# Optimization experiments

Measured on AMD Instinct MI355X. Metric: run time of the kernel, lower is better.

## Reference

```python
import jax, jax.numpy as jnp
import numpy as np

D_MODEL = 1024
N_HEAD = 16
D_HEAD = D_MODEL // N_HEAD
N_EXPERTS = 8
TOP_K = 2
D_FF = 4096
EPS = 1e-6


def setup_inputs() -> dict:
    key = jax.random.key(0)
    ks = jax.random.split(key, 16)
    s = 0.02  # init scale
    d, dff, E = D_MODEL, D_FF, N_EXPERTS
    return {
        "dec": jax.random.normal(ks[0], (4, 1024, d), jnp.float32),
        "text_encoder": jax.random.normal(ks[1], (4, 512, d), jnp.float32),
        # self-attention projections
        "Wq1": jax.random.normal(ks[2], (d, d), jnp.float32) * s,
        "Wk1": jax.random.normal(ks[3], (d, d), jnp.float32) * s,
        "Wv1": jax.random.normal(ks[4], (d, d), jnp.float32) * s,
        "Wo1": jax.random.normal(ks[5], (d, d), jnp.float32) * s,
        # cross-attention projections
        "Wq2": jax.random.normal(ks[6], (d, d), jnp.float32) * s,
        "Wk2": jax.random.normal(ks[7], (d, d), jnp.float32) * s,
        "Wv2": jax.random.normal(ks[8], (d, d), jnp.float32) * s,
        "Wo2": jax.random.normal(ks[9], (d, d), jnp.float32) * s,
        # shared RMSNorm gain (module uses one norm instance three times)
        "g": jnp.ones((d,), jnp.float32),
        # MoE router + per-expert FFN weights
        "Wg": jax.random.normal(ks[10], (d, E), jnp.float32) * s,
        "W1": jax.random.normal(ks[11], (E, d, dff), jnp.float32) * s,
        "W2": jax.random.normal(ks[12], (E, dff, d), jnp.float32) * s,
    }


def rmsnorm(x, g):
    return x * jax.lax.rsqrt(jnp.mean(x * x, axis=-1, keepdims=True) + EPS) * g


def mha(q_in, k_in, v_in, Wq, Wk, Wv, Wo):
    B, Sq, _ = q_in.shape
    Sk = k_in.shape[1]
    q = (q_in @ Wq).reshape(B, Sq, N_HEAD, D_HEAD)
    k = (k_in @ Wk).reshape(B, Sk, N_HEAD, D_HEAD)
    v = (v_in @ Wv).reshape(B, Sk, N_HEAD, D_HEAD)
    scores = jnp.einsum("bqhd,bkhd->bhqk", q, k) / jnp.sqrt(jnp.asarray(D_HEAD, q.dtype))
    attn = jax.nn.softmax(scores, axis=-1)
    out = jnp.einsum("bhqk,bkhd->bqhd", attn, v).reshape(B, Sq, D_MODEL)
    return out @ Wo


def moe(x, Wg, W1, W2):
    # top-k softmax router, renormalized weights; dense per-expert FFN with combine
    probs = jax.nn.softmax(x @ Wg, axis=-1)              # [B,S,E]
    weights, indices = jax.lax.top_k(probs, TOP_K)        # [B,S,k]
    weights = weights / jnp.sum(weights, axis=-1, keepdims=True)
    # combine[t,e] = sum_k weights[t,k] * (indices[t,k]==e)
    combine = jnp.sum(
        jax.nn.one_hot(indices, N_EXPERTS, dtype=x.dtype) * weights[..., None], axis=-2
    )  # [B,S,E]
    out = jnp.zeros_like(x)
    for e in range(N_EXPERTS):  # fixed small expert loop
        h = jax.nn.relu(x @ W1[e]) @ W2[e]
        out = out + combine[..., e:e + 1] * h
    return weights, indices, out


def reference(dec, text_encoder, Wq1, Wk1, Wv1, Wo1, Wq2, Wk2, Wv2, Wo2, g, Wg, W1, W2):
    # self-attention + residual + RMSNorm (dropout p=0 -> identity)
    x = rmsnorm(mha(dec, dec, dec, Wq1, Wk1, Wv1, Wo1) + dec, g)
    # cross-attention + residual + RMSNorm
    x = rmsnorm(mha(x, text_encoder, text_encoder, Wq2, Wk2, Wv2, Wo2) + x, g)
    # MoE FFN + residual + RMSNorm
    weights, indices, y = moe(x, Wg, W1, W2)
    x = rmsnorm(y + x, g)
    return weights, indices, x
```

## Files before the change

### kernel.cpp

```cpp
#include <hip/hip_runtime.h>
#include <stdint.h>

#define D_    1024
#define BB    4
#define SDEC  1024
#define STXT  512
#define TDEC  4096
#define TTXT  2048
#define NH    16
#define DHD   64
#define NE    8
#define DFF   4096
#define NSLOT 8192
#define ND1   8192
#define ND2   4096
#define MOEGRID 512

using u16 = unsigned short;
typedef __attribute__((ext_vector_type(8))) short bf16x8;
typedef __attribute__((ext_vector_type(4))) float f32x4;

__device__ __forceinline__ float bf2f(u16 h) {
    union { unsigned int u; float f; } x; x.u = ((unsigned int)h) << 16; return x.f;
}
__device__ __forceinline__ u16 f2bf(float f) {
    union { float f; unsigned int u; } x; x.f = f;
    unsigned int lsb = (x.u >> 16) & 1u;
    return (u16)((x.u + 0x7fffu + lsb) >> 16);
}

__device__ __forceinline__ void gld16(const u16* g, u16* l) {
    __builtin_amdgcn_global_load_lds((const __attribute__((address_space(1))) void*)g,
                                     (__attribute__((address_space(3))) void*)l,
                                     16, 0, 0);
}

template<int EPI>
__global__ __launch_bounds__(256) void proj_k64(
    const u16* __restrict__ AH, const u16* __restrict__ AL,
    const u16* __restrict__ BH, const u16* __restrict__ BL,
    float* __restrict__ Cf, u16* __restrict__ CH, u16* __restrict__ CL,
    int M, int N, int ldc)
{
    __shared__ u16 smem[24576];
    u16* sAH = smem;
    u16* sAL = smem + 8192;
    u16* sBH = smem + 16384;
    u16* sBL = smem + 20480;

    const int tileM = blockIdx.y * 128, tileN = blockIdx.x * 64;
    const int t = threadIdx.x;
    const int srow = t >> 3;
    const int scol = ((t & 7) ^ (srow & 7)) << 3;
    const u16* pA  = AH + (long)(tileM + srow) * 1024 + scol;
    const u16* pAl = AL + (long)(tileM + srow) * 1024 + scol;
    const u16* pB  = BH + (long)(tileN + srow) * 1024 + scol;
    const u16* pBl = BL + (long)(tileN + srow) * 1024 + scol;

    const int lane = t & 63, wv = t >> 6;
    const int wr = wv << 5;
    const int fr = lane & 15, kg = lane >> 4;

    f32x4 acc[2][4];
    const f32x4 vzero = {0.f, 0.f, 0.f, 0.f};
#pragma unroll
    for (int m = 0; m < 2; ++m)
#pragma unroll
        for (int n = 0; n < 4; ++n) acc[m][n] = vzero;

    for (int rr = 0; rr < 16; ++rr) {
        const long k0 = (long)rr << 6;
#pragma unroll
        for (int c = 0; c < 4; ++c) {
            const long ro = 32L * c * 1024;
            gld16(pA  + k0 + ro, sAH + c * 2048 + t * 8);
            gld16(pAl + k0 + ro, sAL + c * 2048 + t * 8);
        }
#pragma unroll
        for (int c = 0; c < 2; ++c) {
            const long ro = 32L * c * 1024;
            gld16(pB  + k0 + ro, sBH + c * 2048 + t * 8);
            gld16(pBl + k0 + ro, sBL + c * 2048 + t * 8);
        }
        __syncthreads();

#pragma unroll
        for (int ks = 0; ks < 2; ++ks) {
            bf16x8 fa[2], fb[4], fal[2], fbl[4];
#pragma unroll
            for (int m = 0; m < 2; ++m) {
                const int r = wr + m * 16 + fr;
                const int o = r * 64 + (((kg | (ks << 2)) ^ (r & 7)) << 3);
                fa[m]  = *(const bf16x8*)&sAH[o];
                fal[m] = *(const bf16x8*)&sAL[o];
            }
#pragma unroll
            for (int n = 0; n < 4; ++n) {
                const int r = n * 16 + fr;
                const int o = r * 64 + (((kg | (ks << 2)) ^ (r & 7)) << 3);
                fb[n]  = *(const bf16x8*)&sBH[o];
                fbl[n] = *(const bf16x8*)&sBL[o];
            }
#pragma unroll
            for (int m = 0; m < 2; ++m)
#pragma unroll
                for (int n = 0; n < 4; ++n) {
                    acc[m][n] = __builtin_amdgcn_mfma_f32_16x16x32_bf16(fa[m],  fb[n],  acc[m][n], 0, 0, 0);
                    acc[m][n] = __builtin_amdgcn_mfma_f32_16x16x32_bf16(fa[m],  fbl[n], acc[m][n], 0, 0, 0);
                    acc[m][n] = __builtin_amdgcn_mfma_f32_16x16x32_bf16(fal[m], fb[n],  acc[m][n], 0, 0, 0);
                }
        }
        __syncthreads();
    }

#pragma unroll
    for (int m = 0; m < 2; ++m) {
        const int r0 = tileM + wr + m * 16 + (kg << 2);
#pragma unroll
        for (int n = 0; n < 4; ++n) {
            const int col = tileN + n * 16 + fr;
#pragma unroll
            for (int i = 0; i < 4; ++i) {
                const float v = acc[m][n][i];
                const long off = (long)(r0 + i) * ldc + col;
                if constexpr (EPI == 0) {
                    Cf[off] = v;
                } else {
                    const u16 h = f2bf(v);
                    CH[off] = h;
                    CL[off] = f2bf(v - bf2f(h));
                }
            }
        }
    }
}

__global__ __launch_bounds__(256) void scores_k64(
    const u16* __restrict__ AH, const u16* __restrict__ AL,
    const u16* __restrict__ BH, const u16* __restrict__ BL,
    u16* __restrict__ CH, u16* __restrict__ CL,
    int lda, int ldb, int ldc, int nb2,
    long strA1, long strA2, long strB1, long strB2, long strC1, long strC2)
{
    __shared__ u16 smem[4 * 8192];
    u16* sAH = smem;
    u16* sAL = smem + 8192;
    u16* sBH = smem + 16384;
    u16* sBL = smem + 24576;

    const int z = blockIdx.z;
    const int z1 = z / nb2, z2 = z % nb2;
    const long zA = (long)z1 * strA1 + (long)z2 * strA2;
    const long zB = (long)z1 * strB1 + (long)z2 * strB2;
    const long zC = (long)z1 * strC1 + (long)z2 * strC2;

    const int tileM = blockIdx.y * 128, tileN = blockIdx.x * 128;
    const int t = threadIdx.x;
    const int srow = t >> 3;
    const int scol = ((t & 7) ^ (srow & 7)) << 3;
    const u16* pA  = AH + zA + (long)(tileM + srow) * lda + scol;
    const u16* pAl = AL + zA + (long)(tileM + srow) * lda + scol;
    const u16* pB  = BH + zB + (long)(tileN + srow) * ldb + scol;
    const u16* pBl = BL + zB + (long)(tileN + srow) * ldb + scol;

#pragma unroll
    for (int c = 0; c < 4; ++c) {
        const long ro = 32L * c * lda;
        const long rb = 32L * c * ldb;
        gld16(pA  + ro, sAH + c * 2048 + t * 8);
        gld16(pAl + ro, sAL + c * 2048 + t * 8);
        gld16(pB  + rb, sBH + c * 2048 + t * 8);
        gld16(pBl + rb, sBL + c * 2048 + t * 8);
    }
    __syncthreads();

    const int lane = t & 63;
    const int wv = t >> 6;
    const int wr = (wv >> 1) << 6, wc = (wv & 1) << 6;
    const int fr = lane & 15, kg = lane >> 4;

    f32x4 acc[4][4];
    const f32x4 vzero = {0.f, 0.f, 0.f, 0.f};
#pragma unroll
    for (int m = 0; m < 4; ++m)
#pragma unroll
        for (int n = 0; n < 4; ++n) acc[m][n] = vzero;

#pragma unroll
    for (int ks = 0; ks < 2; ++ks) {
        bf16x8 fa[4], fb[4], fal[4], fbl[4];
#pragma unroll
        for (int m = 0; m < 4; ++m) {
            const int r = wr + m * 16 + fr;
            const int o = r * 64 + (((kg | (ks << 2)) ^ (r & 7)) << 3);
            fa[m]  = *(const bf16x8*)&sAH[o];
            fal[m] = *(const bf16x8*)&sAL[o];
        }
#pragma unroll
        for (int n = 0; n < 4; ++n) {
            const int r = wc + n * 16 + fr;
            const int o = r * 64 + (((kg | (ks << 2)) ^ (r & 7)) << 3);
            fb[n]  = *(const bf16x8*)&sBH[o];
            fbl[n] = *(const bf16x8*)&sBL[o];
        }
#pragma unroll
        for (int m = 0; m < 4; ++m)
#pragma unroll
            for (int n = 0; n < 4; ++n) {
                acc[m][n] = __builtin_amdgcn_mfma_f32_16x16x32_bf16(fa[m],  fb[n],  acc[m][n], 0, 0, 0);
                acc[m][n] = __builtin_amdgcn_mfma_f32_16x16x32_bf16(fa[m],  fbl[n], acc[m][n], 0, 0, 0);
                acc[m][n] = __builtin_amdgcn_mfma_f32_16x16x32_bf16(fal[m], fb[n],  acc[m][n], 0, 0, 0);
            }
    }

#pragma unroll
    for (int m = 0; m < 4; ++m) {
        const int r0 = tileM + wr + m * 16 + (kg << 2);
#pragma unroll
        for (int n = 0; n < 4; ++n) {
            const int col = tileN + wc + n * 16 + fr;
#pragma unroll
            for (int i = 0; i < 4; ++i) {
                const float v = acc[m][n][i];
                const long off = zC + (long)(r0 + i) * ldc + col;
                const u16 h = f2bf(v);
                CH[off] = h;
                CL[off] = f2bf(v - bf2f(h));
            }
        }
    }
}

__global__ __launch_bounds__(256) void pv_k64(
    const u16* __restrict__ PHp, const u16* __restrict__ PLp,
    const u16* __restrict__ VTH, const u16* __restrict__ VTL,
    float* __restrict__ Op, int Skv, int NZ)
{
    __shared__ u16 smem[24576];
    u16* sAH = smem;
    u16* sAL = smem + 8192;
    u16* sBH = smem + 16384;
    u16* sBL = smem + 20480;

    const int kq = blockIdx.x;
    const int tileM = blockIdx.y * 128;
    const int z = blockIdx.z;
    const int kbase = kq * (Skv >> 2);
    const int nrounds = Skv >> 8;

    const int t = threadIdx.x;
    const int srow = t >> 3;
    const int scol = ((t & 7) ^ (srow & 7)) << 3;
    const u16* pA  = PHp + (long)z * 1024 * Skv + (long)(tileM + srow) * Skv + kbase + scol;
    const u16* pAl = PLp + (long)z * 1024 * Skv + (long)(tileM + srow) * Skv + kbase + scol;
    const u16* pB  = VTH + (long)z * 64 * Skv + (long)srow * Skv + kbase + scol;
    const u16* pBl = VTL + (long)z * 64 * Skv + (long)srow * Skv + kbase + scol;

    const int lane = t & 63, wv = t >> 6;
    const int wr = wv << 5;
    const int fr = lane & 15, kg = lane >> 4;

    f32x4 acc[2][4];
    const f32x4 vzero = {0.f, 0.f, 0.f, 0.f};
#pragma unroll
    for (int m = 0; m < 2; ++m)
#pragma unroll
        for (int n = 0; n < 4; ++n) acc[m][n] = vzero;

    for (int rr = 0; rr < nrounds; ++rr) {
        const long k0 = (long)rr << 6;
#pragma unroll
        for (int c = 0; c < 4; ++c) {
            const long ro = 32L * c * Skv;
            gld16(pA  + k0 + ro, sAH + c * 2048 + t * 8);
            gld16(pAl + k0 + ro, sAL + c * 2048 + t * 8);
        }
#pragma unroll
        for (int c = 0; c < 2; ++c) {
            const long ro = 32L * c * Skv;
            gld16(pB  + k0 + ro, sBH + c * 2048 + t * 8);
            gld16(pBl + k0 + ro, sBL + c * 2048 + t * 8);
        }
        __syncthreads();

#pragma unroll
        for (int ks = 0; ks < 2; ++ks) {
            bf16x8 fa[2], fb[4], fal[2], fbl[4];
#pragma unroll
            for (int m = 0; m < 2; ++m) {
                const int r = wr + m * 16 + fr;
                const int o = r * 64 + (((kg | (ks << 2)) ^ (r & 7)) << 3);
                fa[m]  = *(const bf16x8*)&sAH[o];
                fal[m] = *(const bf16x8*)&sAL[o];
            }
#pragma unroll
            for (int n = 0; n < 4; ++n) {
                const int r = n * 16 + fr;
                const int o = r * 64 + (((kg | (ks << 2)) ^ (r & 7)) << 3);
                fb[n]  = *(const bf16x8*)&sBH[o];
                fbl[n] = *(const bf16x8*)&sBL[o];
            }
#pragma unroll
            for (int m = 0; m < 2; ++m)
#pragma unroll
                for (int n = 0; n < 4; ++n) {
                    acc[m][n] = __builtin_amdgcn_mfma_f32_16x16x32_bf16(fa[m],  fb[n],  acc[m][n], 0, 0, 0);
                    acc[m][n] = __builtin_amdgcn_mfma_f32_16x16x32_bf16(fa[m],  fbl[n], acc[m][n], 0, 0, 0);
                    acc[m][n] = __builtin_amdgcn_mfma_f32_16x16x32_bf16(fal[m], fb[n],  acc[m][n], 0, 0, 0);
                }
        }
        __syncthreads();
    }

    const long base = ((long)kq * NZ + z) * 65536;
#pragma unroll
    for (int m = 0; m < 2; ++m) {
        const int r0 = tileM + wr + m * 16 + (kg << 2);
#pragma unroll
        for (int n = 0; n < 4; ++n) {
            const int col = n * 16 + fr;
#pragma unroll
            for (int i = 0; i < 4; ++i)
                Op[base + (long)(r0 + i) * 64 + col] = acc[m][n][i];
        }
    }
}

__global__ __launch_bounds__(256) void pv_combine(
    const float* __restrict__ Op, u16* __restrict__ aoH, u16* __restrict__ aoL,
    int nz, int nh)
{
    const long i = ((long)blockIdx.x * 256 + threadIdx.x) * 4;
    const int zz = (int)(i >> 16);
    const int rem = (int)(i & 65535);
    const int r = rem >> 6, c = rem & 63;
    const int b = zz / nh, h = zz % nh;
    const long kqS = (long)nz * 65536;
    float4 v = *(const float4*)(Op + i);
    const float4 v1 = *(const float4*)(Op + kqS + i);
    const float4 v2 = *(const float4*)(Op + 2 * kqS + i);
    const float4 v3 = *(const float4*)(Op + 3 * kqS + i);
    v.x += v1.x + v2.x + v3.x;
    v.y += v1.y + v2.y + v3.y;
    v.z += v1.z + v2.z + v3.z;
    v.w += v1.w + v2.w + v3.w;
    const long dst = (long)b * SDEC * D_ + (long)r * D_ + h * 64 + c;
    u16 h0 = f2bf(v.x), h1 = f2bf(v.y), h2 = f2bf(v.z), h3 = f2bf(v.w);
    uint2 hh;
    hh.x = (unsigned)h0 | ((unsigned)h1 << 16);
    hh.y = (unsigned)h2 | ((unsigned)h3 << 16);
    *(uint2*)(aoH + dst) = hh;
    u16 l0 = f2bf(v.x - bf2f(h0)), l1 = f2bf(v.y - bf2f(h1));
    u16 l2 = f2bf(v.z - bf2f(h2)), l3 = f2bf(v.w - bf2f(h3));
    uint2 ll;
    ll.x = (unsigned)l0 | ((unsigned)l1 << 16);
    ll.y = (unsigned)l2 | ((unsigned)l3 << 16);
    *(uint2*)(aoL + dst) = ll;
}

template<int EPI>
__global__ __launch_bounds__(256, 2) void moe_gemm2(
    const u16* __restrict__ Ag, int lda,
    const u16* __restrict__ BTbase, int ldb, long btStride,
    float* __restrict__ Cf0, float* __restrict__ Cf1, u16* __restrict__ CH, int ldc,
    const int4* __restrict__ desc, int ndesc, int Kiter)
{
    __shared__ u16 smem[32768];
    const int t = threadIdx.x;
    const int lane = t & 63, wv = t >> 6;
    const int wr = (wv >> 1) << 6, wc = (wv & 1) << 6;
    const int fr = lane & 15, kg = lane >> 4;
    const int nks = Kiter >> 5;

    const int rS = t >> 2;
    const int cS = ((t & 3) ^ ((t >> 3) & 3)) << 3;

    int ldsA[4], ldsB[4];
#pragma unroll
    for (int m = 0; m < 4; ++m) {
        const int ra = wr + m * 16 + fr;
        ldsA[m] = ra * 32 + ((kg ^ ((ra >> 1) & 3)) << 3);
        const int rb = wc + m * 16 + fr;
        ldsB[m] = rb * 32 + ((kg ^ ((rb >> 1) & 3)) << 3);
    }

    for (int p = blockIdx.x; p < ndesc; p += MOEGRID) {
        const int4 d = desc[p];
        if (d.x < 0) continue;
        const int rowbase = d.x, colbase = d.y & 0xFFFF, e = d.y >> 16;
        const int kbase = d.z, s1 = d.w;
        const u16* paS = Ag + (long)(rowbase + rS) * lda + kbase + cS;
        const u16* pbS = BTbase + (long)e * btStride + (long)(colbase + rS) * ldb + kbase + cS;
        const long hA = 64L * lda, hB = 64L * ldb;

        f32x4 acc[4][4];
        const f32x4 vzero = {0.f, 0.f, 0.f, 0.f};
#pragma unroll
        for (int m = 0; m < 4; ++m)
#pragma unroll
            for (int n = 0; n < 4; ++n) acc[m][n] = vzero;

#define STG(ks) { const int s_ = (ks) & 3; const long k0_ = (long)(ks) << 5; \
        u16* b_ = smem + s_ * 8192; \
        gld16(paS + k0_,      b_ + t * 8); \
        gld16(paS + k0_ + hA, b_ + 2048 + t * 8); \
        gld16(pbS + k0_,      b_ + 4096 + t * 8); \
        gld16(pbS + k0_ + hB, b_ + 6144 + t * 8); }

        STG(0); STG(1); STG(2);
        asm volatile("s_waitcnt vmcnt(8)" ::: "memory");
        __builtin_amdgcn_s_barrier();
        __builtin_amdgcn_sched_barrier(0);

        for (int ks = 0; ks < nks; ++ks) {
            if (ks + 3 < nks) STG(ks + 3);
            const u16* sA = smem + (ks & 3) * 8192;
            const u16* sB = sA + 4096;
            bf16x8 fa[4], fb[4];
#pragma unroll
            for (int m = 0; m < 4; ++m) fa[m] = *(const bf16x8*)&sA[ldsA[m]];
#pragma unroll
            for (int n = 0; n < 4; ++n) fb[n] = *(const bf16x8*)&sB[ldsB[n]];
            __builtin_amdgcn_s_setprio(1);
#pragma unroll
            for (int m = 0; m < 4; ++m)
#pragma unroll
                for (int n = 0; n < 4; ++n)
                    acc[m][n] = __builtin_amdgcn_mfma_f32_16x16x32_bf16(fa[m], fb[n], acc[m][n], 0, 0, 0);
            __builtin_amdgcn_s_setprio(0);
            if (ks + 3 < nks)      { asm volatile("s_waitcnt vmcnt(8)" ::: "memory"); }
            else if (ks + 2 < nks) { asm volatile("s_waitcnt vmcnt(4)" ::: "memory"); }
            else                   { asm volatile("s_waitcnt vmcnt(0)" ::: "memory"); }
            __builtin_amdgcn_s_barrier();
            __builtin_amdgcn_sched_barrier(0);
        }
#undef STG

        float* __restrict__ C = (EPI == 0) ? ((kbase == 0) ? Cf0 : Cf1) : nullptr;
#pragma unroll
        for (int m = 0; m < 4; ++m) {
            const int r0 = rowbase + wr + m * 16 + (kg << 2);
#pragma unroll
            for (int n = 0; n < 4; ++n) {
                const int col = colbase + wc + n * 16 + fr;
#pragma unroll
                for (int i = 0; i < 4; ++i) {
                    const int r = r0 + i;
                    if (r >= s1) continue;
                    const float v = acc[m][n][i];
                    const long off = (long)r * ldc + col;
                    if constexpr (EPI == 0) C[off] = v;
                    else                    CH[off] = f2bf(fmaxf(v, 0.f));
                }
            }
        }
    }
}

__global__ __launch_bounds__(256) void split2k(const float* __restrict__ in,
                                               u16* __restrict__ oh, u16* __restrict__ ol, long n)
{
    long i = ((long)blockIdx.x * 256 + threadIdx.x) * 4;
    if (i >= n) return;
    float4 v = *(const float4*)(in + i);
    u16 h0 = f2bf(v.x), h1 = f2bf(v.y), h2 = f2bf(v.z), h3 = f2bf(v.w);
    uint2 oo;
    oo.x = (unsigned)h0 | ((unsigned)h1 << 16);
    oo.y = (unsigned)h2 | ((unsigned)h3 << 16);
    *(uint2*)(oh + i) = oo;
    if (ol) {
        u16 l0 = f2bf(v.x - bf2f(h0)), l1 = f2bf(v.y - bf2f(h1));
        u16 l2 = f2bf(v.z - bf2f(h2)), l3 = f2bf(v.w - bf2f(h3));
        uint2 ll;
        ll.x = (unsigned)l0 | ((unsigned)l1 << 16);
        ll.y = (unsigned)l2 | ((unsigned)l3 << 16);
        *(uint2*)(ol + i) = ll;
    }
}

struct Ptr8 { const float* p[8]; };
__global__ __launch_bounds__(256) void transpose_split_w(
    Ptr8 in, u16* __restrict__ oh, u16* __restrict__ ol)
{
    __shared__ float tile[32][33];
    const int z = blockIdx.z;
    const float* ip = in.p[z];
    u16* ohp = oh + (long)z * D_ * D_;
    u16* olp = ol + (long)z * D_ * D_;
    const int c0 = blockIdx.x * 32, r0 = blockIdx.y * 32;
    const int tx = threadIdx.x & 31, ty = threadIdx.x >> 5;
    for (int i = ty; i < 32; i += 8)
        tile[i][tx] = ip[(long)(r0 + i) * D_ + c0 + tx];
    __syncthreads();
    for (int i = ty; i < 32; i += 8) {
        int oc = c0 + i, orr = r0 + tx;
        float v = tile[tx][i];
        u16 h = f2bf(v);
        ohp[(long)oc * D_ + orr] = h;
        olp[(long)oc * D_ + orr] = f2bf(v - bf2f(h));
    }
}

__global__ __launch_bounds__(256) void transpose_split(
    const float* __restrict__ in, u16* __restrict__ oh, u16* __restrict__ ol,
    int R, int C, int ild, long ibs1, long ibs2, int nb2, int old_, long obs)
{
    __shared__ float tile[32][33];
    const int z = blockIdx.z;
    const float* ip = in + (long)(z / nb2) * ibs1 + (long)(z % nb2) * ibs2;
    u16* ohp = oh + (long)z * obs;
    u16* olp = ol ? ol + (long)z * obs : nullptr;
    const int c0 = blockIdx.x * 32, r0 = blockIdx.y * 32;
    const int tx = threadIdx.x & 31, ty = threadIdx.x >> 5;
    for (int i = ty; i < 32; i += 8) {
        int r = r0 + i, c = c0 + tx;
        tile[i][tx] = (r < R && c < C) ? ip[(long)r * ild + c] : 0.f;
    }
    __syncthreads();
    for (int i = ty; i < 32; i += 8) {
        int oc = c0 + i, orr = r0 + tx;
        if (oc < C && orr < R) {
            float v = tile[tx][i];
            u16 h = f2bf(v);
            ohp[(long)oc * old_ + orr] = h;
            if (olp) olp[(long)oc * old_ + orr] = f2bf(v - bf2f(h));
        }
    }
}

__global__ __launch_bounds__(256) void transpose_split_hl(
    const u16* __restrict__ inH, const u16* __restrict__ inL,
    u16* __restrict__ oh, u16* __restrict__ ol,
    int R, int C, int ild, long ibs1, long ibs2, int nb2, int old_, long obs)
{
    __shared__ float tile[32][33];
    const int z = blockIdx.z;
    const long base = (long)(z / nb2) * ibs1 + (long)(z % nb2) * ibs2;
    u16* ohp = oh + (long)z * obs;
    u16* olp = ol + (long)z * obs;
    const int c0 = blockIdx.x * 32, r0 = blockIdx.y * 32;
    const int tx = threadIdx.x & 31, ty = threadIdx.x >> 5;
    for (int i = ty; i < 32; i += 8) {
        int r = r0 + i, c = c0 + tx;
        float v = 0.f;
        if (r < R && c < C) {
            const long o = base + (long)r * ild + c;
            v = bf2f(inH[o]) + bf2f(inL[o]);
        }
        tile[i][tx] = v;
    }
    __syncthreads();
    for (int i = ty; i < 32; i += 8) {
        int oc = c0 + i, orr = r0 + tx;
        if (oc < C && orr < R) {
            float v = tile[tx][i];
            u16 h = f2bf(v);
            ohp[(long)oc * old_ + orr] = h;
            olp[(long)oc * old_ + orr] = f2bf(v - bf2f(h));
        }
    }
}

__global__ __launch_bounds__(256) void softmax_hl(
    u16* __restrict__ ph, u16* __restrict__ pl, int cols, float scale)
{
    u16* php = ph + (long)blockIdx.x * cols;
    u16* plp = pl + (long)blockIdx.x * cols;
    const int t = threadIdx.x;
    float v[4];
    int vpt;
    if (cols == 1024) {
        vpt = 4;
        uint2 hh = ((const uint2*)php)[t];
        uint2 ll = ((const uint2*)plp)[t];
        v[0] = (bf2f((u16)(hh.x & 0xffff)) + bf2f((u16)(ll.x & 0xffff))) * scale;
        v[1] = (bf2f((u16)(hh.x >> 16))    + bf2f((u16)(ll.x >> 16)))    * scale;
        v[2] = (bf2f((u16)(hh.y & 0xffff)) + bf2f((u16)(ll.y & 0xffff))) * scale;
        v[3] = (bf2f((u16)(hh.y >> 16))    + bf2f((u16)(ll.y >> 16)))    * scale;
    } else {
        vpt = 2;
        unsigned hh = ((const unsigned*)php)[t];
        unsigned ll = ((const unsigned*)plp)[t];
        v[0] = (bf2f((u16)(hh & 0xffff)) + bf2f((u16)(ll & 0xffff))) * scale;
        v[1] = (bf2f((u16)(hh >> 16))    + bf2f((u16)(ll >> 16)))    * scale;
        v[2] = -3.4e38f; v[3] = -3.4e38f;
    }
    float mx = fmaxf(fmaxf(v[0], v[1]), fmaxf(v[2], v[3]));
#pragma unroll
    for (int o = 32; o; o >>= 1) mx = fmaxf(mx, __shfl_xor(mx, o));
    __shared__ float sm[4];
    const int wv = t >> 6, ln = t & 63;
    if (ln == 0) sm[wv] = mx;
    __syncthreads();
    mx = fmaxf(fmaxf(sm[0], sm[1]), fmaxf(sm[2], sm[3]));
    float sum = 0.f;
    for (int i = 0; i < vpt; ++i) { v[i] = expf(v[i] - mx); sum += v[i]; }
#pragma unroll
    for (int o = 32; o; o >>= 1) sum += __shfl_xor(sum, o);
    __shared__ float ss[4];
    if (ln == 0) ss[wv] = sum;
    __syncthreads();
    sum = ss[0] + ss[1] + ss[2] + ss[3];
    const float inv = 1.f / sum;
    if (cols == 1024) {
        float q0 = v[0] * inv, q1 = v[1] * inv, q2 = v[2] * inv, q3 = v[3] * inv;
        u16 h0 = f2bf(q0), h1 = f2bf(q1), h2 = f2bf(q2), h3 = f2bf(q3);
        uint2 hh; hh.x = (unsigned)h0 | ((unsigned)h1 << 16); hh.y = (unsigned)h2 | ((unsigned)h3 << 16);
        ((uint2*)php)[t] = hh;
        u16 l0 = f2bf(q0 - bf2f(h0)), l1 = f2bf(q1 - bf2f(h1));
        u16 l2 = f2bf(q2 - bf2f(h2)), l3 = f2bf(q3 - bf2f(h3));
        uint2 llo; llo.x = (unsigned)l0 | ((unsigned)l1 << 16); llo.y = (unsigned)l2 | ((unsigned)l3 << 16);
        ((uint2*)plp)[t] = llo;
    } else {
        float q0 = v[0] * inv, q1 = v[1] * inv;
        u16 h0 = f2bf(q0), h1 = f2bf(q1);
        ((unsigned*)php)[t] = (unsigned)h0 | ((unsigned)h1 << 16);
        u16 l0 = f2bf(q0 - bf2f(h0)), l1 = f2bf(q1 - bf2f(h1));
        ((unsigned*)plp)[t] = (unsigned)l0 | ((unsigned)l1 << 16);
    }
}

__global__ __launch_bounds__(256) void add_rmsnorm(
    const float* __restrict__ a, const float* __restrict__ b, const float* __restrict__ g,
    float* __restrict__ xo, u16* __restrict__ xh, u16* __restrict__ xl)
{
    const long row = blockIdx.x;
    const int t = threadIdx.x;
    const float* pa = a + row * D_;
    const float* pb = b + row * D_;
    float v[4]; double ssq = 0.0;
#pragma unroll
    for (int i = 0; i < 4; ++i) {
        int c = t + (i << 8);
        v[i] = pa[c] + pb[c];
        ssq += (double)v[i] * v[i];
    }
#pragma unroll
    for (int o = 32; o; o >>= 1) ssq += __shfl_xor(ssq, o);
    __shared__ double sd[4];
    if ((t & 63) == 0) sd[t >> 6] = ssq;
    __syncthreads();
    ssq = sd[0] + sd[1] + sd[2] + sd[3];
    const float rs = (float)(1.0 / sqrt(ssq * (1.0 / 1024.0) + 1e-6));
#pragma unroll
    for (int i = 0; i < 4; ++i) {
        int c = t + (i << 8);
        float o = v[i] * rs * g[c];
        xo[row * D_ + c] = o;
        if (xh) {
            u16 h = f2bf(o);
            xh[row * D_ + c] = h;
            if (xl) xl[row * D_ + c] = f2bf(o - bf2f(h));
        }
    }
}

__global__ __launch_bounds__(256) void router_topk(
    const float* __restrict__ x2, const float* __restrict__ Wg,
    float* __restrict__ outw, float* __restrict__ outi,
    int* __restrict__ idx, float* __restrict__ tokw, int* __restrict__ counts, int T)
{
    const int wid = (int)((blockIdx.x * 256 + threadIdx.x) >> 6);
    const int lane = threadIdx.x & 63;
    if (wid >= T) return;
    float acc[NE];
#pragma unroll
    for (int e = 0; e < NE; ++e) acc[e] = 0.f;
    const float* xr = x2 + (long)wid * D_;
    for (int i = 0; i < 16; ++i) {
        float xv = xr[i * 64 + lane];
        const float* wr = Wg + (long)(i * 64 + lane) * NE;
#pragma unroll
        for (int e = 0; e < NE; ++e) acc[e] += xv * wr[e];
    }
#pragma unroll
    for (int e = 0; e < NE; ++e)
#pragma unroll
        for (int o = 32; o; o >>= 1) acc[e] += __shfl_xor(acc[e], o);
    if (lane == 0) {
        float m = acc[0];
#pragma unroll
        for (int e = 1; e < NE; ++e) m = fmaxf(m, acc[e]);
        float p[NE], s = 0.f;
#pragma unroll
        for (int e = 0; e < NE; ++e) { p[e] = expf(acc[e] - m); s += p[e]; }
        const float invs = 1.f / s;
#pragma unroll
        for (int e = 0; e < NE; ++e) p[e] *= invs;
        int e0 = 0;
#pragma unroll
        for (int e = 1; e < NE; ++e) if (p[e] > p[e0]) e0 = e;
        int e1 = (e0 == 0) ? 1 : 0;
#pragma unroll
        for (int e = 0; e < NE; ++e) if (e != e0 && e != e1 && p[e] > p[e1]) e1 = e;
        float w0 = p[e0], w1 = p[e1];
        const float sw = 1.f / (w0 + w1);
        w0 *= sw; w1 *= sw;
        outw[2 * wid] = w0;      outw[2 * wid + 1] = w1;
        outi[2 * wid] = (float)e0; outi[2 * wid + 1] = (float)e1;
        idx[2 * wid] = e0;       idx[2 * wid + 1] = e1;
        tokw[2 * wid] = w0;      tokw[2 * wid + 1] = w1;
        atomicAdd(&counts[e0], 1);
        atomicAdd(&counts[e1], 1);
    }
}

__global__ void scan_desc(const int* __restrict__ counts, int* __restrict__ cursor,
                          int4* __restrict__ d1, int4* __restrict__ d2)
{
    __shared__ int sseg[NE + 1];
    if (threadIdx.x == 0) {
        int a = 0;
        for (int e = 0; e < NE; ++e) { sseg[e] = a; cursor[e] = a; a += counts[e]; }
        sseg[NE] = a;
    }
    __syncthreads();
    const int e = threadIdx.x;
    if (e < NE) {
        const int s0 = sseg[e], s1 = sseg[e + 1];
        const int nyt = (s1 - s0 + 127) >> 7;
        for (int xt = 0; xt < 32; ++xt)
            for (int yt = 0; yt < nyt; ++yt)
                d1[e + 8 * (xt * nyt + yt)] =
                    make_int4(s0 + yt * 128, (xt * 128) | (e << 16), 0, s1);
        for (int kh = 0; kh < 2; ++kh)
            for (int xt = 0; xt < 8; ++xt)
                for (int yt = 0; yt < nyt; ++yt)
                    d2[e + 8 * ((kh * 8 + xt) * nyt + yt)] =
                        make_int4(s0 + yt * 128, (xt * 128) | (e << 16), kh * 2048, s1);
    }
}

__global__ __launch_bounds__(256) void scatter_slots(
    const int* __restrict__ idx, int* __restrict__ cursor,
    int* __restrict__ row_token, int* __restrict__ slot_of, int T)
{
    const int t = blockIdx.x * 256 + threadIdx.x;
    if (t >= T) return;
#pragma unroll
    for (int k = 0; k < 2; ++k) {
        const int e = idx[2 * t + k];
        const int pos = atomicAdd(&cursor[e], 1);
        row_token[pos] = t;
        slot_of[2 * t + k] = pos;
    }
}

__global__ __launch_bounds__(256) void gather_bf16(
    const float* __restrict__ x2, const int* __restrict__ row_token, u16* __restrict__ Xg)
{
    const int r = blockIdx.x;
    const int t = threadIdx.x;
    const float* src = x2 + (long)row_token[r] * D_ + t * 4;
    float4 v = *(const float4*)src;
    uint2 oo;
    oo.x = (unsigned)f2bf(v.x) | ((unsigned)f2bf(v.y) << 16);
    oo.y = (unsigned)f2bf(v.z) | ((unsigned)f2bf(v.w) << 16);
    *(uint2*)(Xg + (long)r * D_ + t * 4) = oo;
}

__global__ __launch_bounds__(256) void combine_rmsnorm(
    const float* __restrict__ Y0, const float* __restrict__ Y1,
    const int* __restrict__ slot_of, const float* __restrict__ tokw,
    const float* __restrict__ x2, const float* __restrict__ g, float* __restrict__ out)
{
    const long tr = blockIdx.x;
    const int t = threadIdx.x;
    const int s0 = slot_of[2 * tr], s1 = slot_of[2 * tr + 1];
    const float w0 = tokw[2 * tr], w1 = tokw[2 * tr + 1];
    const float* ya0 = Y0 + (long)s0 * D_;
    const float* yb0 = Y1 + (long)s0 * D_;
    const float* ya1 = Y0 + (long)s1 * D_;
    const float* yb1 = Y1 + (long)s1 * D_;
    const float* xr = x2 + tr * D_;
    float v[4]; double ssq = 0.0;
#pragma unroll
    for (int i = 0; i < 4; ++i) {
        int c = t + (i << 8);
        v[i] = w0 * (ya0[c] + yb0[c]) + w1 * (ya1[c] + yb1[c]) + xr[c];
        ssq += (double)v[i] * v[i];
    }
#pragma unroll
    for (int o = 32; o; o >>= 1) ssq += __shfl_xor(ssq, o);
    __shared__ double sd[4];
    if ((t & 63) == 0) sd[t >> 6] = ssq;
    __syncthreads();
    ssq = sd[0] + sd[1] + sd[2] + sd[3];
    const float rs = (float)(1.0 / sqrt(ssq * (1.0 / 1024.0) + 1e-6));
#pragma unroll
    for (int i = 0; i < 4; ++i) {
        int c = t + (i << 8);
        out[tr * D_ + c] = v[i] * rs * g[c];
    }
}

__global__ void sentinel(float* o) { o[0] = 12345.0f; }

extern "C" void kernel_launch(void* const* d_in, const int* in_sizes, int n_in,
                              void* d_out, int out_size, void* d_ws, size_t ws_size,
                              hipStream_t stream)
{
    const float* dec = (const float*)d_in[0];
    const float* te  = (const float*)d_in[1];
    const float* g  = (const float*)d_in[10];
    const float* Wg = (const float*)d_in[11];
    const float* W1 = (const float*)d_in[12];
    const float* W2 = (const float*)d_in[13];
    float* outw = (float*)d_out;
    float* outi = outw + 2 * TDEC;
    float* outx = outw + 4 * TDEC;

    char* ws = (char*)d_ws;
    size_t off = 0;
    auto A = [&](size_t bytes) -> char* {
        char* p = ws + off;
        off += (bytes + 255) & ~(size_t)255;
        return p;
    };

    u16* decH = (u16*)A((size_t)TDEC * D_ * 2);
    u16* decL = (u16*)A((size_t)TDEC * D_ * 2);
    u16* teH  = (u16*)A((size_t)TTXT * D_ * 2);
    u16* teL  = (u16*)A((size_t)TTXT * D_ * 2);
    u16* wtHall = (u16*)A((size_t)8 * D_ * D_ * 2);
    u16* wtLall = (u16*)A((size_t)8 * D_ * D_ * 2);
    float* x1f = (float*)A((size_t)TDEC * D_ * 4);
    float* x2f = (float*)A((size_t)TDEC * D_ * 4);
    float* tokw = (float*)A(NSLOT * 4);
    int* idx    = (int*)A(NSLOT * 4);
    int* counts = (int*)A(256);
    int* cursor = (int*)A(256);
    int* row_token = (int*)A(NSLOT * 4);
    int* slot_of   = (int*)A(NSLOT * 4);
    int4* desc1 = (int4*)A((size_t)ND1 * 16);
    int4* desc2 = (int4*)A((size_t)ND2 * 16);
    const size_t Rbase = off;

    u16* W1T  = (u16*)A((size_t)NE * DFF * D_ * 2);
    u16* W2T  = (u16*)A((size_t)NE * D_ * DFF * 2);
    u16* Xg   = (u16*)A((size_t)(NSLOT + 256) * D_ * 2);
    u16* Hb   = (u16*)A((size_t)(NSLOT + 256) * DFF * 2);
    float* Yseg = (float*)A((size_t)NSLOT * D_ * 4);
    float* Ypart1 = (float*)W1T;
    const size_t moeEnd = off;

    auto allocAttn = [&](bool batched, u16*& PH, u16*& PL, u16*& qkvH, u16*& qkvL,
                         u16*& q2H, u16*& q2L, u16*& kv2H, u16*& kv2L,
                         u16*& vTH, u16*& vTL, u16*& aoH, u16*& aoL,
                         u16*& x1H, u16*& x1L, float*& of, float*& Opart) {
        off = Rbase;
        const size_t pcell = batched ? (size_t)BB * NH * SDEC * SDEC * 2
                                     : (size_t)NH * SDEC * SDEC * 2;
        PH = (u16*)A(pcell);
        PL = (u16*)A(pcell);
        qkvH = (u16*)A((size_t)TDEC * 3 * D_ * 2);
        qkvL = (u16*)A((size_t)TDEC * 3 * D_ * 2);
        q2H  = (u16*)A((size_t)TDEC * D_ * 2);
        q2L  = (u16*)A((size_t)TDEC * D_ * 2);
        kv2H = (u16*)A((size_t)TTXT * 2 * D_ * 2);
        kv2L = (u16*)A((size_t)TTXT * 2 * D_ * 2);
        vTH = (u16*)A((size_t)TDEC * D_ * 2);
        vTL = (u16*)A((size_t)TDEC * D_ * 2);
        aoH = (u16*)A((size_t)TDEC * D_ * 2);
        aoL = (u16*)A((size_t)TDEC * D_ * 2);
        x1H = (u16*)A((size_t)TDEC * D_ * 2);
        x1L = (u16*)A((size_t)TDEC * D_ * 2);
        of  = (float*)A((size_t)TDEC * D_ * 4);
        Opart = (float*)A((size_t)4 * (batched ? BB * NH : NH) * SDEC * DHD * 4);
        return off;
    };

    u16 *PH, *PL, *qkvH, *qkvL, *q2H, *q2L, *kv2H, *kv2L, *vTH, *vTL, *aoH, *aoL, *x1H, *x1L;
    float *of, *Opart;
    size_t attnEnd = allocAttn(true, PH, PL, qkvH, qkvL, q2H, q2L, kv2H, kv2L,
                               vTH, vTL, aoH, aoL, x1H, x1L, of, Opart);
    bool batched = ws_size >= (attnEnd > moeEnd ? attnEnd : moeEnd);
    if (!batched) {
        attnEnd = allocAttn(false, PH, PL, qkvH, qkvL, q2H, q2L, kv2H, kv2L,
                            vTH, vTL, aoH, aoL, x1H, x1L, of, Opart);
        if (ws_size < (attnEnd > moeEnd ? attnEnd : moeEnd)) {
            sentinel<<<1, 1, 0, stream>>>(outw);
            return;
        }
    }

    const dim3 blk(256);

    split2k<<<dim3((TDEC * D_) / 1024), blk, 0, stream>>>(dec, decH, decL, (long)TDEC * D_);
    split2k<<<dim3((TTXT * D_) / 1024), blk, 0, stream>>>(te, teH, teL, (long)TTXT * D_);
    Ptr8 wp;
    for (int i = 0; i < 8; ++i) wp.p[i] = (const float*)d_in[2 + i];
    transpose_split_w<<<dim3(32, 32, 8), blk, 0, stream>>>(wp, wtHall, wtLall);

    proj_k64<1><<<dim3(48, 32), blk, 0, stream>>>(decH, decL, wtHall, wtLall,
        nullptr, qkvH, qkvL, TDEC, 3 * D_, 3 * D_);
    transpose_split_hl<<<dim3(2, 32, BB * NH), blk, 0, stream>>>(qkvH + 2 * D_, qkvL + 2 * D_,
        vTH, vTL, SDEC, DHD, 3 * D_, (long)SDEC * 3 * D_, DHD, NH, SDEC, (long)DHD * SDEC);

    if (batched) {
        scores_k64<<<dim3(8, 8, BB * NH), blk, 0, stream>>>(
            qkvH, qkvL, qkvH + D_, qkvL + D_, PH, PL,
            3 * D_, 3 * D_, SDEC, NH,
            (long)SDEC * 3 * D_, DHD, (long)SDEC * 3 * D_, DHD,
            (long)NH * SDEC * SDEC, (long)SDEC * SDEC);
        softmax_hl<<<dim3(BB * NH * SDEC), blk, 0, stream>>>(PH, PL, SDEC, 0.125f);
        pv_k64<<<dim3(4, 8, BB * NH), blk, 0, stream>>>(PH, PL, vTH, vTL, Opart, SDEC, BB * NH);
        pv_combine<<<dim3(BB * NH * 64), blk, 0, stream>>>(Opart, aoH, aoL, BB * NH, NH);
    } else {
        for (int b = 0; b < BB; ++b) {
            const long qo3 = (long)b * SDEC * 3 * D_;
            const long qo  = (long)b * SDEC * D_;
            scores_k64<<<dim3(8, 8, NH), blk, 0, stream>>>(
                qkvH + qo3, qkvL + qo3, qkvH + qo3 + D_, qkvL + qo3 + D_,
                PH, PL, 3 * D_, 3 * D_, SDEC, NH,
                0, DHD, 0, DHD, 0, (long)SDEC * SDEC);
            softmax_hl<<<dim3(NH * SDEC), blk, 0, stream>>>(PH, PL, SDEC, 0.125f);
            pv_k64<<<dim3(4, 8, NH), blk, 0, stream>>>(PH, PL,
                vTH + (long)b * NH * DHD * SDEC, vTL + (long)b * NH * DHD * SDEC,
                Opart, SDEC, NH);
            pv_combine<<<dim3(NH * 64), blk, 0, stream>>>(Opart, aoH + qo, aoL + qo, NH, NH);
        }
    }
    proj_k64<0><<<dim3(16, 32), blk, 0, stream>>>(aoH, aoL,
        wtHall + (size_t)3 * D_ * D_, wtLall + (size_t)3 * D_ * D_,
        of, nullptr, nullptr, TDEC, D_, D_);
    add_rmsnorm<<<dim3(TDEC), blk, 0, stream>>>(of, dec, g, x1f, x1H, x1L);

    proj_k64<1><<<dim3(16, 32), blk, 0, stream>>>(x1H, x1L,
        wtHall + (size_t)4 * D_ * D_, wtLall + (size_t)4 * D_ * D_,
        nullptr, q2H, q2L, TDEC, D_, D_);
    proj_k64<1><<<dim3(32, 16), blk, 0, stream>>>(teH, teL,
        wtHall + (size_t)5 * D_ * D_, wtLall + (size_t)5 * D_ * D_,
        nullptr, kv2H, kv2L, TTXT, 2 * D_, 2 * D_);
    transpose_split_hl<<<dim3(2, 16, BB * NH), blk, 0, stream>>>(kv2H + D_, kv2L + D_,
        vTH, vTL, STXT, DHD, 2 * D_, (long)STXT * 2 * D_, DHD, NH, STXT, (long)DHD * STXT);

    if (batched) {
        scores_k64<<<dim3(4, 8, BB * NH), blk, 0, stream>>>(
            q2H, q2L, kv2H, kv2L, PH, PL,
            D_, 2 * D_, STXT, NH,
            (long)SDEC * D_, DHD, (long)STXT * 2 * D_, DHD,
            (long)NH * SDEC * STXT, (long)SDEC * STXT);
        softmax_hl<<<dim3(BB * NH * SDEC), blk, 0, stream>>>(PH, PL, STXT, 0.125f);
        pv_k64<<<dim3(4, 8, BB * NH), blk, 0, stream>>>(PH, PL, vTH, vTL, Opart, STXT, BB * NH);
        pv_combine<<<dim3(BB * NH * 64), blk, 0, stream>>>(Opart, aoH, aoL, BB * NH, NH);
    } else {
        for (int b = 0; b < BB; ++b) {
            const long qo  = (long)b * SDEC * D_;
            const long ko2 = (long)b * STXT * 2 * D_;
            scores_k64<<<dim3(4, 8, NH), blk, 0, stream>>>(
                q2H + qo, q2L + qo, kv2H + ko2, kv2L + ko2,
                PH, PL, D_, 2 * D_, STXT, NH,
                0, DHD, 0, DHD, 0, (long)SDEC * STXT);
            softmax_hl<<<dim3(NH * SDEC), blk, 0, stream>>>(PH, PL, STXT, 0.125f);
            pv_k64<<<dim3(4, 8, NH), blk, 0, stream>>>(PH, PL,
                vTH + (long)b * NH * DHD * STXT, vTL + (long)b * NH * DHD * STXT,
                Opart, STXT, NH);
            pv_combine<<<dim3(NH * 64), blk, 0, stream>>>(Opart, aoH + qo, aoL + qo, NH, NH);
        }
    }
    proj_k64<0><<<dim3(16, 32), blk, 0, stream>>>(aoH, aoL,
        wtHall + (size_t)7 * D_ * D_, wtLall + (size_t)7 * D_ * D_,
        of, nullptr, nullptr, TDEC, D_, D_);
    add_rmsnorm<<<dim3(TDEC), blk, 0, stream>>>(of, x1f, g, x2f, nullptr, nullptr);

    hipMemsetAsync(counts, 0, 32, stream);
    hipMemsetAsync(desc1, 0xFF, (size_t)ND1 * 16, stream);
    hipMemsetAsync(desc2, 0xFF, (size_t)ND2 * 16, stream);
    router_topk<<<dim3(TDEC / 4), blk, 0, stream>>>(x2f, Wg, outw, outi, idx, tokw, counts, TDEC);
    scan_desc<<<1, 64, 0, stream>>>(counts, cursor, desc1, desc2);
    scatter_slots<<<dim3(TDEC / 256), blk, 0, stream>>>(idx, cursor, row_token, slot_of, TDEC);
    gather_bf16<<<dim3(NSLOT), blk, 0, stream>>>(x2f, row_token, Xg);

    transpose_split<<<dim3(DFF / 32, D_ / 32, NE), blk, 0, stream>>>(W1, W1T, nullptr,
        D_, DFF, DFF, (long)D_ * DFF, 0, 1, D_, (long)DFF * D_);
    transpose_split<<<dim3(D_ / 32, DFF / 32, NE), blk, 0, stream>>>(W2, W2T, nullptr,
        DFF, D_, D_, (long)D_ * DFF, 0, 1, DFF, (long)D_ * DFF);
    moe_gemm2<2><<<dim3(MOEGRID), blk, 0, stream>>>(Xg, D_, W1T, D_, (long)DFF * D_,
        nullptr, nullptr, Hb, DFF, desc1, ND1, 1024);
    moe_gemm2<0><<<dim3(MOEGRID), blk, 0, stream>>>(Hb, DFF, W2T, DFF, (long)D_ * DFF,
        Yseg, Ypart1, nullptr, D_, desc2, ND2, 2048);
    combine_rmsnorm<<<dim3(TDEC), blk, 0, stream>>>(Yseg, Ypart1, slot_of, tokw, x2f, g, outx);

    (void)in_sizes; (void)n_in; (void)out_size;
}
```

Before: 1.245 ms.

## Replace 4-stage LDS pipeline in MoE GEMM with single-buffer 64-wide K rounds

```diff
diff --git a/kernel.cpp b/kernel.cpp
--- a/kernel.cpp
+++ b/kernel.cpp
@@ -14,7 +14,7 @@
 #define NSLOT 8192
 #define ND1   8192
 #define ND2   4096
-#define MOEGRID 512
+#define MOEGRID 1280
 
 using u16 = unsigned short;
 typedef __attribute__((ext_vector_type(8))) short bf16x8;
@@ -359,39 +359,32 @@
 }
 
 template<int EPI>
-__global__ __launch_bounds__(256, 2) void moe_gemm2(
+__global__ __launch_bounds__(256) void moe_gemm2(
     const u16* __restrict__ Ag, int lda,
     const u16* __restrict__ BTbase, int ldb, long btStride,
     float* __restrict__ Cf0, float* __restrict__ Cf1, u16* __restrict__ CH, int ldc,
     const int4* __restrict__ desc, int ndesc, int Kiter)
 {
-    __shared__ u16 smem[32768];
+    __shared__ u16 smem[16384];
+    u16* sA = smem;
+    u16* sB = smem + 8192;
+
     const int t = threadIdx.x;
     const int lane = t & 63, wv = t >> 6;
     const int wr = (wv >> 1) << 6, wc = (wv & 1) << 6;
     const int fr = lane & 15, kg = lane >> 4;
-    const int nks = Kiter >> 5;
-
-    const int rS = t >> 2;
-    const int cS = ((t & 3) ^ ((t >> 3) & 3)) << 3;
-
-    int ldsA[4], ldsB[4];
-#pragma unroll
-    for (int m = 0; m < 4; ++m) {
-        const int ra = wr + m * 16 + fr;
-        ldsA[m] = ra * 32 + ((kg ^ ((ra >> 1) & 3)) << 3);
-        const int rb = wc + m * 16 + fr;
-        ldsB[m] = rb * 32 + ((kg ^ ((rb >> 1) & 3)) << 3);
-    }
+    const int nrounds = Kiter >> 6;
+
+    const int srow = t >> 3;
+    const int scol = ((t & 7) ^ (srow & 7)) << 3;
 
     for (int p = blockIdx.x; p < ndesc; p += MOEGRID) {
         const int4 d = desc[p];
         if (d.x < 0) continue;
         const int rowbase = d.x, colbase = d.y & 0xFFFF, e = d.y >> 16;
         const int kbase = d.z, s1 = d.w;
-        const u16* paS = Ag + (long)(rowbase + rS) * lda + kbase + cS;
-        const u16* pbS = BTbase + (long)e * btStride + (long)(colbase + rS) * ldb + kbase + cS;
-        const long hA = 64L * lda, hB = 64L * ldb;
+        const u16* pA = Ag + (long)(rowbase + srow) * lda + kbase + scol;
+        const u16* pB = BTbase + (long)e * btStride + (long)(colbase + srow) * ldb + kbase + scol;
 
         f32x4 acc[4][4];
         const f32x4 vzero = {0.f, 0.f, 0.f, 0.f};
@@ -400,41 +393,36 @@
 #pragma unroll
             for (int n = 0; n < 4; ++n) acc[m][n] = vzero;
 
-#define STG(ks) { const int s_ = (ks) & 3; const long k0_ = (long)(ks) << 5; \
-        u16* b_ = smem + s_ * 8192; \
-        gld16(paS + k0_,      b_ + t * 8); \
-        gld16(paS + k0_ + hA, b_ + 2048 + t * 8); \
-        gld16(pbS + k0_,      b_ + 4096 + t * 8); \
-        gld16(pbS + k0_ + hB, b_ + 6144 + t * 8); }
-
-        STG(0); STG(1); STG(2);
-        asm volatile("s_waitcnt vmcnt(8)" ::: "memory");
-        __builtin_amdgcn_s_barrier();
-        __builtin_amdgcn_sched_barrier(0);
-
-        for (int ks = 0; ks < nks; ++ks) {
-            if (ks + 3 < nks) STG(ks + 3);
-            const u16* sA = smem + (ks & 3) * 8192;
-            const u16* sB = sA + 4096;
-            bf16x8 fa[4], fb[4];
-#pragma unroll
-            for (int m = 0; m < 4; ++m) fa[m] = *(const bf16x8*)&sA[ldsA[m]];
-#pragma unroll
-            for (int n = 0; n < 4; ++n) fb[n] = *(const bf16x8*)&sB[ldsB[n]];
-            __builtin_amdgcn_s_setprio(1);
-#pragma unroll
-            for (int m = 0; m < 4; ++m)
-#pragma unroll
-                for (int n = 0; n < 4; ++n)
-                    acc[m][n] = __builtin_amdgcn_mfma_f32_16x16x32_bf16(fa[m], fb[n], acc[m][n], 0, 0, 0);
-            __builtin_amdgcn_s_setprio(0);
-            if (ks + 3 < nks)      { asm volatile("s_waitcnt vmcnt(8)" ::: "memory"); }
-            else if (ks + 2 < nks) { asm volatile("s_waitcnt vmcnt(4)" ::: "memory"); }
-            else                   { asm volatile("s_waitcnt vmcnt(0)" ::: "memory"); }
-            __builtin_amdgcn_s_barrier();
-            __builtin_amdgcn_sched_barrier(0);
-        }
-#undef STG
+        for (int rr = 0; rr < nrounds; ++rr) {
+            const long k0 = (long)rr << 6;
+#pragma unroll
+            for (int c = 0; c < 4; ++c) {
+                gld16(pA + k0 + 32L * c * lda, sA + c * 2048 + t * 8);
+                gld16(pB + k0 + 32L * c * ldb, sB + c * 2048 + t * 8);
+            }
+            __syncthreads();
+
+#pragma unroll
+            for (int ks = 0; ks < 2; ++ks) {
+                bf16x8 fa[4], fb[4];
+#pragma unroll
+                for (int m = 0; m < 4; ++m) {
+                    const int r = wr + m * 16 + fr;
+                    fa[m] = *(const bf16x8*)&sA[r * 64 + (((kg | (ks << 2)) ^ (r & 7)) << 3)];
+                }
+#pragma unroll
+                for (int n = 0; n < 4; ++n) {
+                    const int r = wc + n * 16 + fr;
+                    fb[n] = *(const bf16x8*)&sB[r * 64 + (((kg | (ks << 2)) ^ (r & 7)) << 3)];
+                }
+#pragma unroll
+                for (int m = 0; m < 4; ++m)
+#pragma unroll
+                    for (int n = 0; n < 4; ++n)
+                        acc[m][n] = __builtin_amdgcn_mfma_f32_16x16x32_bf16(fa[m], fb[n], acc[m][n], 0, 0, 0);
+            }
+            __syncthreads();
+        }
 
         float* __restrict__ C = (EPI == 0) ? ((kbase == 0) ? Cf0 : Cf1) : nullptr;
 #pragma unroll
```

After: 1.291 ms. 3.8% more time.
